# Performance work log

Measured on AMD Instinct MI355X. Metric: run time of the kernel, lower is better.

## Reference

```python
import jax, jax.numpy as jnp
import numpy as np

B, DIM, IN_DIM, H, W = 4, 512, 256, 64, 64
DOWN = IN_DIM // 2          # 128
QK = DOWN // 8              # 16
EPS = 1e-5


def conv2d(x, w, b, pad=0, dil=1):
    y = jax.lax.conv_general_dilated(
        x, w, window_strides=(1, 1),
        padding=[(pad, pad), (pad, pad)],
        rhs_dilation=(dil, dil),
        dimension_numbers=('NCHW', 'OIHW', 'NCHW'))
    return y + b[None, :, None, None]


def bn(x, g, bt, m, v):
    # inference-mode BatchNorm2d with running stats
    scale = (g * jax.lax.rsqrt(v + EPS))[None, :, None, None]
    return (x - m[None, :, None, None]) * scale + bt[None, :, None, None]


def prelu(x, a):
    return jnp.where(x >= 0, x, a * x)


def setup_inputs() -> dict:
    key = jax.random.key(0)
    ks = iter(jax.random.split(key, 64))
    d = {}
    d['x'] = jax.random.normal(next(ks), (B, DIM, H, W), dtype=jnp.float32)

    def conv_params(name, cout, cin, k):
        d[name + '_w'] = jax.random.normal(next(ks), (cout, cin, k, k), jnp.float32) * 0.05
        d[name + '_b'] = jax.random.normal(next(ks), (cout,), jnp.float32) * 0.05

    def bn_params(name, c):
        d[name + '_g'] = 1.0 + 0.1 * jax.random.normal(next(ks), (c,), jnp.float32)
        d[name + '_bt'] = 0.1 * jax.random.normal(next(ks), (c,), jnp.float32)
        d[name + '_m'] = 0.1 * jax.random.normal(next(ks), (c,), jnp.float32)
        d[name + '_v'] = 0.5 + jax.random.uniform(next(ks), (c,), jnp.float32)

    def prelu_param(name):
        d[name] = jnp.full((1,), 0.25, jnp.float32)

    conv_params('dc', IN_DIM, DIM, 3);  bn_params('dc_bn', IN_DIM); prelu_param('dc_a')
    conv_params('c1', DOWN, IN_DIM, 1); bn_params('c1_bn', DOWN);   prelu_param('c1_a')
    conv_params('c2', DOWN, IN_DIM, 3); bn_params('c2_bn', DOWN);   prelu_param('c2_a')
    conv_params('q', QK, DOWN, 1)
    conv_params('k', QK, DOWN, 1)
    conv_params('v', DOWN, DOWN, 1)
    d['gamma2'] = jnp.full((1,), 0.1, jnp.float32)  # torch init is 0; nonzero to exercise the path
    conv_params('c3', DOWN, IN_DIM, 1); bn_params('c3_bn', DOWN);   prelu_param('c3_a')
    conv_params('f', IN_DIM, 3 * DOWN, 1); bn_params('f_bn', IN_DIM); prelu_param('f_a')
    return d


def reference(x,
              dc_w, dc_b, dc_bn_g, dc_bn_bt, dc_bn_m, dc_bn_v, dc_a,
              c1_w, c1_b, c1_bn_g, c1_bn_bt, c1_bn_m, c1_bn_v, c1_a,
              c2_w, c2_b, c2_bn_g, c2_bn_bt, c2_bn_m, c2_bn_v, c2_a,
              q_w, q_b, k_w, k_b, v_w, v_b, gamma2,
              c3_w, c3_b, c3_bn_g, c3_bn_bt, c3_bn_m, c3_bn_v, c3_a,
              f_w, f_b, f_bn_g, f_bn_bt, f_bn_m, f_bn_v, f_a):
    # down_conv: 3x3 conv + BN + PReLU
    x = prelu(bn(conv2d(x, dc_w, dc_b, pad=1), dc_bn_g, dc_bn_bt, dc_bn_m, dc_bn_v), dc_a)
    # branch 1: 1x1 conv
    c1 = prelu(bn(conv2d(x, c1_w, c1_b), c1_bn_g, c1_bn_bt, c1_bn_m, c1_bn_v), c1_a)
    # branch 2: dilated 3x3 conv + non-local self-attention
    c2 = prelu(bn(conv2d(x, c2_w, c2_b, pad=2, dil=2), c2_bn_g, c2_bn_bt, c2_bn_m, c2_bn_v), c2_a)
    b, c, h, w = c2.shape
    hw = h * w
    q = conv2d(c2, q_w, q_b).reshape(b, QK, hw)   # [B, C/8, HW]
    k = conv2d(c2, k_w, k_b).reshape(b, QK, hw)
    v = conv2d(c2, v_w, v_b).reshape(b, c, hw)
    energy = jnp.einsum('bcn,bcm->bnm', q, k)     # [B, HW, HW]
    attn = jax.nn.softmax(energy, axis=-1)
    out2 = jnp.einsum('bcm,bnm->bcn', v, attn).reshape(b, c, h, w)
    out2 = gamma2 * out2 + c2
    # branch 3: global avg pool -> 1x1 conv -> broadcast (bilinear upsample of 1x1 is constant)
    pooled = jnp.mean(x, axis=(2, 3), keepdims=True)  # [B, IN_DIM, 1, 1]
    c3 = prelu(bn(conv2d(pooled, c3_w, c3_b), c3_bn_g, c3_bn_bt, c3_bn_m, c3_bn_v), c3_a)
    c3 = jnp.broadcast_to(c3, (b, DOWN, h, w))
    # fuse
    cat = jnp.concatenate([c1, out2, c3], axis=1)
    return prelu(bn(conv2d(cat, f_w, f_b), f_bn_g, f_bn_bt, f_bn_m, f_bn_v), f_a)
```

## Files before the change

kernel.cpp:

```cpp
#include <hip/hip_runtime.h>
#include <hip/hip_bf16.h>
#include <math.h>

#define HW 4096
#define EPSV 1e-5f

typedef unsigned short ushort;
typedef __attribute__((ext_vector_type(8))) short bf16x8;
typedef __attribute__((ext_vector_type(4))) float f32x4;

__device__ inline ushort f2bf(float f) {
    __hip_bfloat16 h = __float2bfloat16(f);
    return *reinterpret_cast<ushort*>(&h);
}
__device__ inline float bf2f(ushort u) {
    unsigned int v = ((unsigned int)u) << 16;
    return __uint_as_float(v);
}

template<int C>
__global__ __launch_bounds__(256) void to_chlast_bf16(
    const float* __restrict__ src, ushort* __restrict__ dst)
{
    const int b = blockIdx.z, c0 = blockIdx.y * 64, p0 = blockIdx.x * 64;
    const int tid = threadIdx.x;
    __shared__ float sT[64][65];
    for (int i = tid; i < 4096; i += 256) {
        const int ch = i >> 6, px = i & 63;
        sT[ch][px] = src[(size_t)(b * C + c0 + ch) * HW + p0 + px];
    }
    __syncthreads();
    const int px = tid >> 2, seg = tid & 3;
    ushort tmp[16];
    #pragma unroll
    for (int j = 0; j < 16; ++j) tmp[j] = f2bf(sT[seg * 16 + j][px]);
    ushort* d = dst + (size_t)(b * HW + p0 + px) * C + c0 + seg * 16;
    *(uint4*)d = *(uint4*)&tmp[0];
    *(uint4*)(d + 8) = *(uint4*)&tmp[8];
}

__global__ __launch_bounds__(256) void dc_combine(
    const float* __restrict__ part,
    const float* __restrict__ bias, const float* __restrict__ bng,
    const float* __restrict__ bnb, const float* __restrict__ bnm,
    const float* __restrict__ bnv, const float* __restrict__ al,
    ushort* __restrict__ dst)
{
    const int b = blockIdx.z, c0 = blockIdx.y * 64, p0 = blockIdx.x * 64;
    const int tid = threadIdx.x;
    __shared__ float sT[64][65];
    __shared__ float sSc[64], sSh[64];
    if (tid < 64) {
        const int c = c0 + tid;
        const float sc = bng[c] * rsqrtf(bnv[c] + EPSV);
        sSc[tid] = sc;
        sSh[tid] = (bias[c] - bnm[c]) * sc + bnb[c];
    }
    __syncthreads();
    const float a = al[0];
    for (int i = tid; i < 4096; i += 256) {
        const int ch = i >> 6, px = i & 63;
        const size_t i0 = (size_t)(b * 256 + c0 + ch) * HW + p0 + px;
        float v = part[i0] + part[i0 + (size_t)4 * 256 * HW];
        float t = v * sSc[ch] + sSh[ch];
        sT[ch][px] = t >= 0.f ? t : a * t;
    }
    __syncthreads();
    const int px = tid >> 2, seg = tid & 3;
    ushort tmp[16];
    #pragma unroll
    for (int j = 0; j < 16; ++j) tmp[j] = f2bf(sT[seg * 16 + j][px]);
    ushort* d = dst + (size_t)(b * HW + p0 + px) * 256 + c0 + seg * 16;
    *(uint4*)d = *(uint4*)&tmp[0];
    *(uint4*)(d + 8) = *(uint4*)&tmp[8];
}

template<int KS>
__global__ __launch_bounds__(256) void c2_combine(
    const float* __restrict__ part,
    const float* __restrict__ bias, const float* __restrict__ bng,
    const float* __restrict__ bnb, const float* __restrict__ bnm,
    const float* __restrict__ bnv, const float* __restrict__ al,
    float* __restrict__ out)
{
    const int c = blockIdx.y, b = blockIdx.z;
    const int px = blockIdx.x * 1024 + threadIdx.x * 4;
    const float sc = bng[c] * rsqrtf(bnv[c] + EPSV);
    const float sh = (bias[c] - bnm[c]) * sc + bnb[c];
    const float a = al[0];
    const size_t i0 = (size_t)(b * 128 + c) * HW + px;
    float4 s = {0.f, 0.f, 0.f, 0.f};
    #pragma unroll
    for (int k = 0; k < KS; ++k) {
        const float4 v = *(const float4*)&part[i0 + (size_t)k * 4 * 128 * HW];
        s.x += v.x; s.y += v.y; s.z += v.z; s.w += v.w;
    }
    float4 o;
    float t;
    t = s.x * sc + sh; o.x = t >= 0.f ? t : a * t;
    t = s.y * sc + sh; o.y = t >= 0.f ? t : a * t;
    t = s.z * sc + sh; o.z = t >= 0.f ? t : a * t;
    t = s.w * sc + sh; o.w = t >= 0.f ? t : a * t;
    *(float4*)&out[(size_t)(b * 128 + c) * HW + px] = o;
}

template<int CIN, int COUT>
__global__ __launch_bounds__(256) void pack_w3x3(
    const float* __restrict__ w, ushort* __restrict__ wpk)
{
    const int idx = blockIdx.x * 256 + threadIdx.x;
    constexpr int total = 9 * (CIN / 32) * COUT * 32;
    if (idx >= total) return;
    const int ci_in = idx & 31;
    int rest = idx >> 5;
    const int co = rest % COUT; rest /= COUT;
    const int cc = rest % (CIN / 32);
    const int tap = rest / (CIN / 32);
    wpk[idx] = f2bf(w[((size_t)co * CIN + cc * 32 + ci_in) * 9 + tap]);
}

__global__ __launch_bounds__(256) void pack_w1x1(
    const float* __restrict__ w, ushort* __restrict__ o,
    int K, int stride, int total)
{
    const int idx = blockIdx.x * 256 + threadIdx.x;
    if (idx >= total) return;
    const int co = idx / K, k = idx - co * K;
    o[idx] = f2bf(w[(size_t)co * stride + k]);
}

template<int CIN, int COUT, int COTILE, int DIL, int ROWS, int KS>
__global__ __launch_bounds__(256, 2) void conv3x3_mfma(
    const ushort* __restrict__ xin,
    const ushort* __restrict__ wpk,
    float* __restrict__ outp)
{
    constexpr int HR = ROWS + 2 * DIL;
    constexpr int NC = 64 + 2 * DIL;
    constexpr int MT = COTILE / 16;
    constexpr int WPR = 4 / ROWS;
    constexpr int NT = ROWS;
    constexpr int SAS = 40;
    constexpr int NCO = COUT / COTILE;
    constexpr int CH = CIN / 32 / KS;
    constexpr int NA = HR * NC * 4;
    constexpr int NREG = (NA + 255) / 256;
    constexpr int WCH = 9 * MT * 64;
    constexpr int WPT = (WCH + 255) / 256;

    const int tid = threadIdx.x;
    const int wave = tid >> 6, lane = tid & 63;
    const int l15 = lane & 15, quad = lane >> 4;
    const int b = blockIdx.z;
    const int cob = blockIdx.y % NCO;
    const int ks = blockIdx.y / NCO;
    const int co0 = cob * COTILE;
    const int h0 = blockIdx.x * ROWS;
    const int row = wave / WPR;
    const int ntbase = (wave % WPR) * NT;

    __shared__ __align__(16) ushort sA[HR * NC * SAS];
    __shared__ __align__(16) ushort sW[WCH * 8];

    f32x4 acc[MT][NT];
    #pragma unroll
    for (int mt = 0; mt < MT; ++mt)
        #pragma unroll
        for (int nt = 0; nt < NT; ++nt) acc[mt][nt] = (f32x4){0.f, 0.f, 0.f, 0.f};

    uint4 xreg[NREG];
    uint4 wreg[WPT];

    auto loadx = [&](int cc) {
        #pragma unroll
        for (int k = 0; k < NREG; ++k) {
            const int i = tid + k * 256;
            uint4 val = {0u, 0u, 0u, 0u};
            if (i < NA) {
                const int p = i >> 2, seg = i & 3;
                const int r = p / NC, c = p - r * NC;
                const int grow = h0 - DIL + r, gcol = c - DIL;
                if (grow >= 0 && grow < 64 && gcol >= 0 && gcol < 64)
                    val = *(const uint4*)&xin[((size_t)(b * 64 + grow) * 64 + gcol) * CIN
                                              + cc * 32 + seg * 8];
            }
            xreg[k] = val;
        }
    };
    auto loadw = [&](int cc) {
        #pragma unroll
        for (int k = 0; k < WPT; ++k) {
            const int i = tid + k * 256;
            if (i < WCH) {
                const int tap = i / (MT * 64);
                const int r = i - tap * (MT * 64);
                const int mt = r >> 6, n = r & 63;
                wreg[k] = *(const uint4*)&wpk[
                    ((size_t)(tap * (CIN / 32) + cc) * COUT + co0 + mt * 16 + (n & 15)) * 32
                    + (n >> 4) * 8];
            }
        }
    };

    loadx(ks * CH);
    loadw(ks * CH);

    #pragma unroll 1
    for (int cc = ks * CH; cc < (ks + 1) * CH; ++cc) {
        if (cc != ks * CH) __syncthreads();
        #pragma unroll
        for (int k = 0; k < NREG; ++k) {
            const int i = tid + k * 256;
            if (i < NA) *(uint4*)&sA[(i >> 2) * SAS + (i & 3) * 8] = xreg[k];
        }
        #pragma unroll
        for (int k = 0; k < WPT; ++k) {
            const int i = tid + k * 256;
            if (i < WCH) *(uint4*)&sW[i * 8] = wreg[k];
        }
        __syncthreads();

        if (cc + 1 < (ks + 1) * CH) {
            loadx(cc + 1);
            loadw(cc + 1);
        }

        #pragma unroll
        for (int tap = 0; tap < 9; ++tap) {
            const int ty = tap / 3, tx = tap - ty * 3;
            const int rl = row + ty * DIL;
            bf16x8 wf[MT];
            #pragma unroll
            for (int mt = 0; mt < MT; ++mt)
                wf[mt] = *(const bf16x8*)&sW[((tap * MT + mt) * 64 + lane) * 8];
            #pragma unroll
            for (int nt = 0; nt < NT; ++nt) {
                const int cl = (ntbase + nt) * 16 + l15 + tx * DIL;
                const bf16x8 bp = *(const bf16x8*)&sA[(rl * NC + cl) * SAS + quad * 8];
                #pragma unroll
                for (int mt = 0; mt < MT; ++mt)
                    acc[mt][nt] = __builtin_amdgcn_mfma_f32_16x16x32_bf16(
                        wf[mt], bp, acc[mt][nt], 0, 0, 0);
            }
        }
    }

    #pragma unroll
    for (int mt = 0; mt < MT; ++mt)
        #pragma unroll
        for (int rr = 0; rr < 4; ++rr) {
            const int co = co0 + mt * 16 + quad * 4 + rr;
            #pragma unroll
            for (int nt = 0; nt < NT; ++nt)
                outp[((size_t)((ks * 4 + b) * COUT + co) * 64 + h0 + row) * 64
                     + (ntbase + nt) * 16 + l15] = acc[mt][nt][rr];
        }
}

template<int CIN, int COUT, bool BNACT, int OMODE>
__global__ __launch_bounds__(256) void gemm1x1_cl(
    const ushort* __restrict__ xin,
    const ushort* __restrict__ wbf,
    const float* __restrict__ bias, const float* __restrict__ bng,
    const float* __restrict__ bnb, const float* __restrict__ bnm,
    const float* __restrict__ bnv, const float* __restrict__ al,
    const float* __restrict__ ebias, void* __restrict__ outv,
    int ostride, int ocol)
{
    const int tid = threadIdx.x;
    const int wave = tid >> 6, lane = tid & 63;
    const int l15 = lane & 15, quad = lane >> 4;
    const int pix0 = blockIdx.x * 128 + wave * 32;
    const int co0 = blockIdx.y * 64;

    f32x4 acc[4][2];
    #pragma unroll
    for (int mt = 0; mt < 4; ++mt)
        #pragma unroll
        for (int nt = 0; nt < 2; ++nt) acc[mt][nt] = (f32x4){0.f, 0.f, 0.f, 0.f};

    #pragma unroll 2
    for (int cc = 0; cc < CIN / 32; ++cc) {
        bf16x8 aw[4], bp[2];
        #pragma unroll
        for (int mt = 0; mt < 4; ++mt)
            aw[mt] = *(const bf16x8*)&wbf[(size_t)(co0 + mt * 16 + l15) * CIN + cc * 32 + quad * 8];
        #pragma unroll
        for (int nt = 0; nt < 2; ++nt)
            bp[nt] = *(const bf16x8*)&xin[(size_t)(pix0 + nt * 16 + l15) * CIN + cc * 32 + quad * 8];
        #pragma unroll
        for (int mt = 0; mt < 4; ++mt)
            #pragma unroll
            for (int nt = 0; nt < 2; ++nt)
                acc[mt][nt] = __builtin_amdgcn_mfma_f32_16x16x32_bf16(
                    aw[mt], bp[nt], acc[mt][nt], 0, 0, 0);
    }

    const int bI = pix0 >> 12;
    const float a = BNACT ? al[0] : 0.f;

    if (OMODE == 0) {
        float* out = (float*)outv;
        #pragma unroll
        for (int mt = 0; mt < 4; ++mt)
            #pragma unroll
            for (int r = 0; r < 4; ++r) {
                const int co = co0 + mt * 16 + quad * 4 + r;
                float bb = bias[co];
                if (ebias) bb += ebias[bI * COUT + co];
                float scale = 1.f, shift = bb;
                if (BNACT) {
                    scale = bng[co] * rsqrtf(bnv[co] + EPSV);
                    shift = bb * scale + (bnb[co] - bnm[co] * scale);
                }
                #pragma unroll
                for (int nt = 0; nt < 2; ++nt) {
                    float t = acc[mt][nt][r] * scale + shift;
                    if (BNACT) t = t >= 0.f ? t : a * t;
                    out[((size_t)(bI * COUT + co)) * HW + (pix0 & 4095) + nt * 16 + l15] = t;
                }
            }
    } else {
        __shared__ ushort sT[4][32][68];
        #pragma unroll
        for (int mt = 0; mt < 4; ++mt)
            #pragma unroll
            for (int r = 0; r < 4; ++r) {
                const int co = co0 + mt * 16 + quad * 4 + r;
                float bb = bias[co];
                float scale = 1.f, shift = bb;
                if (BNACT) {
                    scale = bng[co] * rsqrtf(bnv[co] + EPSV);
                    shift = bb * scale + (bnb[co] - bnm[co] * scale);
                }
                #pragma unroll
                for (int nt = 0; nt < 2; ++nt) {
                    float t = acc[mt][nt][r] * scale + shift;
                    if (BNACT) t = t >= 0.f ? t : a * t;
                    sT[wave][nt * 16 + l15][mt * 16 + quad * 4 + r] = f2bf(t);
                }
            }
        __syncthreads();
        const int p = lane >> 1, half = lane & 1;
        ushort* out = (ushort*)outv;
        #pragma unroll
        for (int seg = 0; seg < 4; ++seg) {
            uint2 a0 = *(uint2*)&sT[wave][p][half * 32 + seg * 8];
            uint2 a1 = *(uint2*)&sT[wave][p][half * 32 + seg * 8 + 4];
            uint4 vv = {a0.x, a0.y, a1.x, a1.y};
            *(uint4*)&out[(size_t)(pix0 + p) * ostride + ocol + co0 + half * 32 + seg * 8] = vv;
        }
    }
}

template<int CIN, bool BNACT, bool OUTBF16>
__global__ __launch_bounds__(256) void conv1x1_kernel(
    const float* __restrict__ in0,
    const float* __restrict__ wgt, int wstride, int COUT,
    const float* __restrict__ bias, const float* __restrict__ al,
    void* __restrict__ outv)
{
    const int tid = threadIdx.x;
    const int b = blockIdx.z, co0 = blockIdx.y * 64, p0 = blockIdx.x * 64;
    const int cg = tid >> 4, pg = tid & 15;
    const int c0l = cg * 4, w0 = pg * 4;

    __shared__ __align__(16) float sIn[16 * 64];
    __shared__ __align__(16) float sW[16 * 68];

    float acc[4][4] = {};

    for (int cc = 0; cc < CIN; cc += 16) {
        {
            int i = tid;
            #pragma unroll
            for (int it = 0; it < 4; ++it, i += 256) {
                const int px = i & 63, ci = i >> 6;
                sIn[ci * 64 + px] = in0[(size_t)(b * CIN + cc + ci) * HW + p0 + px];
            }
            i = tid;
            #pragma unroll
            for (int it = 0; it < 4; ++it, i += 256) {
                const int ci = i & 15, co = i >> 4;
                sW[ci * 68 + co] = wgt[(co0 + co) * wstride + cc + ci];
            }
        }
        __syncthreads();
        #pragma unroll
        for (int ci = 0; ci < 16; ++ci) {
            const float4 iv = *(const float4*)&sIn[ci * 64 + w0];
            const float4 wv = *(const float4*)&sW[ci * 68 + c0l];
            const float ia[4] = {iv.x, iv.y, iv.z, iv.w};
            const float wa[4] = {wv.x, wv.y, wv.z, wv.w};
            #pragma unroll
            for (int i2 = 0; i2 < 4; ++i2)
                #pragma unroll
                for (int j = 0; j < 4; ++j)
                    acc[i2][j] = fmaf(wa[i2], ia[j], acc[i2][j]);
        }
        __syncthreads();
    }

    const float a = BNACT ? al[0] : 0.f;
    #pragma unroll
    for (int i2 = 0; i2 < 4; ++i2) {
        const int co = co0 + c0l + i2;
        const float shift = bias[co];
        float r[4];
        #pragma unroll
        for (int j = 0; j < 4; ++j) {
            float t = acc[i2][j] + shift;
            r[j] = (BNACT && t < 0.f) ? a * t : t;
        }
        const size_t base = (size_t)(b * COUT + co) * HW + p0 + w0;
        if (OUTBF16) {
            ushort* out = (ushort*)outv;
            #pragma unroll
            for (int j = 0; j < 4; ++j) out[base + j] = f2bf(r[j]);
        } else {
            float* out = (float*)outv;
            *(float4*)&out[base] = make_float4(r[0], r[1], r[2], r[3]);
        }
    }
}

__global__ __launch_bounds__(256) void qk_kernel(
    const float* __restrict__ c2g, const float* __restrict__ qw,
    const float* __restrict__ qb2, const float* __restrict__ kw,
    const float* __restrict__ kb2, ushort* __restrict__ qpack,
    ushort* __restrict__ kpack)
{
    const int b = blockIdx.y, p0 = blockIdx.x * 64, tid = threadIdx.x;
    __shared__ float sC[128][64];
    __shared__ float sWq[16][128];
    __shared__ float sWk[16][128];
    for (int i = tid; i < 8192; i += 256) {
        const int px = i & 63, ci = i >> 6;
        sC[ci][px] = c2g[(size_t)(b * 128 + ci) * HW + p0 + px];
    }
    for (int i = tid; i < 2048; i += 256) {
        const int ci = i & 127, co = i >> 7;
        sWq[co][ci] = qw[co * 128 + ci];
        sWk[co][ci] = kw[co * 128 + ci];
    }
    __syncthreads();
    const int px = tid & 63, grp = tid >> 6;
    const int co0 = (grp & 1) * 8;
    const bool isK = grp >= 2;
    const float* sWp = isK ? &sWk[0][0] : &sWq[0][0];
    float acc[8] = {};
    for (int ci = 0; ci < 128; ++ci) {
        const float xv = sC[ci][px];
        #pragma unroll
        for (int j = 0; j < 8; ++j)
            acc[j] = fmaf(sWp[(co0 + j) * 128 + ci], xv, acc[j]);
    }
    const float* bsrc = isK ? kb2 : qb2;
    ushort* osrc = isK ? kpack : qpack;
    const size_t base = (size_t)(b * 4096 + p0 + px) * 32;
    #pragma unroll
    for (int j = 0; j < 8; ++j) {
        osrc[base + co0 + j] = f2bf(acc[j] + bsrc[co0 + j]);
        osrc[base + 16 + co0 + j] = 0;
    }
}

__global__ __launch_bounds__(256) void attn_flash(
    const ushort* __restrict__ qpack,
    const ushort* __restrict__ kpack,
    const ushort* __restrict__ vpackT,
    ushort* __restrict__ opart,
    float* __restrict__ Mpart,
    float* __restrict__ Spart)
{
    const int tid = threadIdx.x;
    const int wave = tid >> 6, lane = tid & 63;
    const int l15 = lane & 15, quad = lane >> 4;
    const int b = blockIdx.z, j = blockIdx.y;
    const int n0w = blockIdx.x * 128 + wave * 32;
    const int m_begin = j * 512;

    __shared__ __align__(16) ushort sV[2][128][40];
    __shared__ __align__(16) ushort sP[4][2][16][40];

    const bf16x8 bq0 = *(const bf16x8*)(qpack + ((size_t)(b * 4096 + n0w + l15) * 32 + quad * 8));
    const bf16x8 bq1 = *(const bf16x8*)(qpack + ((size_t)(b * 4096 + n0w + 16 + l15) * 32 + quad * 8));
    const f32x4 z = {0.f, 0.f, 0.f, 0.f};

    float runM0 = -3e30f, runM1 = -3e30f;
    #pragma unroll 2
    for (int t = 0; t < 8; ++t) {
        const int m0 = m_begin + t * 64;
        #pragma unroll
        for (int ms = 0; ms < 4; ++ms) {
            const bf16x8 ak = *(const bf16x8*)(
                kpack + ((size_t)(b * 4096 + m0 + ms * 16 + l15) * 32 + quad * 8));
            const f32x4 s0 = __builtin_amdgcn_mfma_f32_16x16x32_bf16(ak, bq0, z, 0, 0, 0);
            const f32x4 s1 = __builtin_amdgcn_mfma_f32_16x16x32_bf16(ak, bq1, z, 0, 0, 0);
            runM0 = fmaxf(runM0, fmaxf(fmaxf(s0[0], s0[1]), fmaxf(s0[2], s0[3])));
            runM1 = fmaxf(runM1, fmaxf(fmaxf(s1[0], s1[1]), fmaxf(s1[2], s1[3])));
        }
    }
    runM0 = fmaxf(runM0, __shfl_xor(runM0, 16));
    runM0 = fmaxf(runM0, __shfl_xor(runM0, 32));
    runM1 = fmaxf(runM1, __shfl_xor(runM1, 16));
    runM1 = fmaxf(runM1, __shfl_xor(runM1, 32));
    const float Ms0 = runM0 * 1.44269504f;
    const float Ms1 = runM1 * 1.44269504f;

    float runS0 = 0.f, runS1 = 0.f;
    f32x4 oacc0[8], oacc1[8];
    #pragma unroll
    for (int cs = 0; cs < 8; ++cs) {
        oacc0[cs] = (f32x4){0.f, 0.f, 0.f, 0.f};
        oacc1[cs] = (f32x4){0.f, 0.f, 0.f, 0.f};
    }

    const int stc = tid >> 1, stseg = tid & 1;

    {
        uint4 v0 = *(const uint4*)&vpackT[(size_t)(b * 128 + stc) * HW + m_begin + stseg * 16];
        uint4 v1 = *(const uint4*)&vpackT[(size_t)(b * 128 + stc) * HW + m_begin + stseg * 16 + 8];
        *(uint4*)&sV[0][stc][stseg * 16] = v0;
        *(uint4*)&sV[0][stc][stseg * 16 + 8] = v1;
    }
    __syncthreads();

    #pragma unroll 1
    for (int t = 0; t < 16; ++t) {
        const int m0 = m_begin + t * 32;
        const int buf = t & 1;
        uint4 nv0, nv1;
        const bool more = (t + 1 < 16);
        if (more) {
            const size_t nb = (size_t)(b * 128 + stc) * HW + m0 + 32 + stseg * 16;
            nv0 = *(const uint4*)&vpackT[nb];
            nv1 = *(const uint4*)&vpackT[nb + 8];
        }
        f32x4 s0[2], s1[2];
        #pragma unroll
        for (int ms = 0; ms < 2; ++ms) {
            const bf16x8 ak = *(const bf16x8*)(
                kpack + ((size_t)(b * 4096 + m0 + ms * 16 + l15) * 32 + quad * 8));
            s0[ms] = __builtin_amdgcn_mfma_f32_16x16x32_bf16(ak, bq0, z, 0, 0, 0);
            s1[ms] = __builtin_amdgcn_mfma_f32_16x16x32_bf16(ak, bq1, z, 0, 0, 0);
        }
        #pragma unroll
        for (int ms = 0; ms < 2; ++ms) {
            float p0[4], p1[4];
            #pragma unroll
            for (int r = 0; r < 4; ++r) {
                p0[r] = __builtin_amdgcn_exp2f(fmaf(s0[ms][r], 1.44269504f, -Ms0));
                p1[r] = __builtin_amdgcn_exp2f(fmaf(s1[ms][r], 1.44269504f, -Ms1));
                runS0 += p0[r];
                runS1 += p1[r];
            }
            ushort4 u0, u1;
            u0.x = f2bf(p0[0]); u0.y = f2bf(p0[1]); u0.z = f2bf(p0[2]); u0.w = f2bf(p0[3]);
            u1.x = f2bf(p1[0]); u1.y = f2bf(p1[1]); u1.z = f2bf(p1[2]); u1.w = f2bf(p1[3]);
            *(uint2*)&sP[wave][0][l15][ms * 16 + quad * 4] = *(uint2*)&u0;
            *(uint2*)&sP[wave][1][l15][ms * 16 + quad * 4] = *(uint2*)&u1;
        }
        asm volatile("s_waitcnt lgkmcnt(0)" ::: "memory");
        const bf16x8 ap0 = *(const bf16x8*)&sP[wave][0][l15][quad * 8];
        const bf16x8 ap1 = *(const bf16x8*)&sP[wave][1][l15][quad * 8];
        #pragma unroll
        for (int cs = 0; cs < 8; ++cs) {
            const bf16x8 bv = *(const bf16x8*)&sV[buf][cs * 16 + l15][quad * 8];
            oacc0[cs] = __builtin_amdgcn_mfma_f32_16x16x32_bf16(ap0, bv, oacc0[cs], 0, 0, 0);
            oacc1[cs] = __builtin_amdgcn_mfma_f32_16x16x32_bf16(ap1, bv, oacc1[cs], 0, 0, 0);
        }
        if (more) {
            *(uint4*)&sV[buf ^ 1][stc][stseg * 16] = nv0;
            *(uint4*)&sV[buf ^ 1][stc][stseg * 16 + 8] = nv1;
            __syncthreads();
        }
    }

    runS0 += __shfl_xor(runS0, 16);
    runS0 += __shfl_xor(runS0, 32);
    runS1 += __shfl_xor(runS1, 16);
    runS1 += __shfl_xor(runS1, 32);
    if (lane < 32) {
        const float Mv = (lane < 16) ? runM0 : runM1;
        const float Sv = (lane < 16) ? runS0 : runS1;
        const int n = n0w + ((lane < 16) ? 0 : 16) + l15;
        Mpart[((size_t)b * 8 + j) * 4096 + n] = Mv;
        Spart[((size_t)b * 8 + j) * 4096 + n] = Sv;
    }
    #pragma unroll
    for (int cs = 0; cs < 8; ++cs)
        #pragma unroll
        for (int r = 0; r < 4; ++r) {
            const int n = n0w + quad * 4 + r;
            opart[(((size_t)b * 8 + j) * 4096 + n) * 128 + cs * 16 + l15] = f2bf(oacc0[cs][r]);
            opart[(((size_t)b * 8 + j) * 4096 + n + 16) * 128 + cs * 16 + l15] = f2bf(oacc1[cs][r]);
        }
}

__global__ __launch_bounds__(256) void attn_combine(
    const ushort* __restrict__ opart, const float* __restrict__ Mpart,
    const float* __restrict__ Spart, const float* __restrict__ c2g,
    const float* __restrict__ gamma2, ushort* __restrict__ catb)
{
    const int b = blockIdx.y, n0 = blockIdx.x * 32, tid = threadIdx.x;
    __shared__ float sC2[128][33];
    __shared__ float sWj[8][32];
    if (tid < 32) {
        const int n = n0 + tid;
        float Mj[8], Sj[8];
        #pragma unroll
        for (int j = 0; j < 8; ++j) {
            Mj[j] = Mpart[((size_t)b * 8 + j) * 4096 + n];
            Sj[j] = Spart[((size_t)b * 8 + j) * 4096 + n];
        }
        float M = -3e30f;
        #pragma unroll
        for (int j = 0; j < 8; ++j) M = fmaxf(M, Mj[j]);
        float St = 0.f, e[8];
        #pragma unroll
        for (int j = 0; j < 8; ++j) { e[j] = __expf(Mj[j] - M); St += Sj[j] * e[j]; }
        const float inv = 1.0f / St;
        #pragma unroll
        for (int j = 0; j < 8; ++j) sWj[j][tid] = e[j] * inv;
    }
    #pragma unroll
    for (int e = 0; e < 16; ++e) {
        const int idx = tid + e * 256;
        const int c = idx >> 5, n = idx & 31;
        sC2[c][n] = c2g[(size_t)(b * 128 + c) * HW + n0 + n];
    }
    __syncthreads();
    const float g2 = gamma2[0];
    #pragma unroll
    for (int e = 0; e < 16; ++e) {
        const int idx = tid + e * 256;
        const int n = idx >> 7, c = idx & 127;
        float s = 0.f;
        #pragma unroll
        for (int j = 0; j < 8; ++j)
            s += bf2f(opart[(((size_t)b * 8 + j) * 4096 + n0 + n) * 128 + c]) * sWj[j][n];
        catb[(size_t)(b * 4096 + n0 + n) * 256 + 128 + c] = f2bf(fmaf(g2, s, sC2[c][n]));
    }
}

__global__ __launch_bounds__(256) void pool_kernel(
    const float* __restrict__ part,
    const float* __restrict__ bias, const float* __restrict__ bng,
    const float* __restrict__ bnb, const float* __restrict__ bnm,
    const float* __restrict__ bnv, const float* __restrict__ al,
    float* __restrict__ pool)
{
    const int c = blockIdx.x, b = blockIdx.y, tid = threadIdx.x;
    const float sc = bng[c] * rsqrtf(bnv[c] + EPSV);
    const float sh = (bias[c] - bnm[c]) * sc + bnb[c];
    const float a = al[0];
    const float4* r0 = (const float4*)(part + (size_t)(b * 256 + c) * HW);
    const float4* r1 = (const float4*)(part + (size_t)((4 + b) * 256 + c) * HW);
    float s = 0.f;
    #pragma unroll 4
    for (int i = tid; i < 1024; i += 256) {
        const float4 t0 = r0[i];
        const float4 t1 = r1[i];
        float v, t;
        v = t0.x + t1.x; t = v * sc + sh; s += t >= 0.f ? t : a * t;
        v = t0.y + t1.y; t = v * sc + sh; s += t >= 0.f ? t : a * t;
        v = t0.z + t1.z; t = v * sc + sh; s += t >= 0.f ? t : a * t;
        v = t0.w + t1.w; t = v * sc + sh; s += t >= 0.f ? t : a * t;
    }
    __shared__ float red[256];
    red[tid] = s; __syncthreads();
    for (int st = 128; st > 0; st >>= 1) {
        if (tid < st) red[tid] += red[tid + st];
        __syncthreads();
    }
    if (tid == 0) pool[b * 256 + c] = red[0] * (1.0f / 4096.0f);
}

__global__ __launch_bounds__(256) void c3_fbias_kernel(
    const float* __restrict__ pool, const float* __restrict__ c3w,
    const float* __restrict__ c3b, const float* __restrict__ bng,
    const float* __restrict__ bnb, const float* __restrict__ bnm,
    const float* __restrict__ bnv, const float* __restrict__ al,
    const float* __restrict__ fw, float* __restrict__ fbias)
{
    const int b = blockIdx.x, tid = threadIdx.x;
    __shared__ float sp[256];
    __shared__ float sc3[128];
    sp[tid] = pool[b * 256 + tid];
    __syncthreads();
    if (tid < 128) {
        float acc = c3b[tid];
        for (int ci = 0; ci < 256; ++ci) acc = fmaf(c3w[tid * 256 + ci], sp[ci], acc);
        const float scale = bng[tid] * rsqrtf(bnv[tid] + EPSV);
        float t = (acc - bnm[tid]) * scale + bnb[tid];
        const float a = al[0];
        sc3[tid] = t >= 0.f ? t : a * t;
    }
    __syncthreads();
    float f = 0.f;
    for (int j = 0; j < 128; ++j) f = fmaf(fw[tid * 384 + 256 + j], sc3[j], f);
    fbias[b * 256 + tid] = f;
}

extern "C" void kernel_launch(void* const* d_in, const int* in_sizes, int n_in,
                              void* d_out, int out_size, void* d_ws, size_t ws_size,
                              hipStream_t stream)
{
    const float* x     = (const float*)d_in[0];
    const float* dc_w  = (const float*)d_in[1];
    const float* dc_b  = (const float*)d_in[2];
    const float* dc_g  = (const float*)d_in[3];
    const float* dc_bt = (const float*)d_in[4];
    const float* dc_m  = (const float*)d_in[5];
    const float* dc_v  = (const float*)d_in[6];
    const float* dc_a  = (const float*)d_in[7];
    const float* c1_w  = (const float*)d_in[8];
    const float* c1_b  = (const float*)d_in[9];
    const float* c1_g  = (const float*)d_in[10];
    const float* c1_bt = (const float*)d_in[11];
    const float* c1_m  = (const float*)d_in[12];
    const float* c1_v  = (const float*)d_in[13];
    const float* c1_a  = (const float*)d_in[14];
    const float* c2_w  = (const float*)d_in[15];
    const float* c2_b  = (const float*)d_in[16];
    const float* c2_g  = (const float*)d_in[17];
    const float* c2_bt = (const float*)d_in[18];
    const float* c2_m  = (const float*)d_in[19];
    const float* c2_v  = (const float*)d_in[20];
    const float* c2_a  = (const float*)d_in[21];
    const float* q_w   = (const float*)d_in[22];
    const float* q_b   = (const float*)d_in[23];
    const float* k_w   = (const float*)d_in[24];
    const float* k_b   = (const float*)d_in[25];
    const float* v_w   = (const float*)d_in[26];
    const float* v_b   = (const float*)d_in[27];
    const float* gamma2= (const float*)d_in[28];
    const float* c3_w  = (const float*)d_in[29];
    const float* c3_b  = (const float*)d_in[30];
    const float* c3_g  = (const float*)d_in[31];
    const float* c3_bt = (const float*)d_in[32];
    const float* c3_m  = (const float*)d_in[33];
    const float* c3_v  = (const float*)d_in[34];
    const float* c3_a  = (const float*)d_in[35];
    const float* f_w   = (const float*)d_in[36];
    const float* f_b   = (const float*)d_in[37];
    const float* f_g   = (const float*)d_in[38];
    const float* f_bt  = (const float*)d_in[39];
    const float* f_m   = (const float*)d_in[40];
    const float* f_v   = (const float*)d_in[41];
    const float* f_a   = (const float*)d_in[42];

    char* base = (char*)d_ws;
    ushort* xbf   = (ushort*)base;
    float*  dcp   = (float*)(base + 16777216);
    float*  c2p   = (float*)base;
    ushort* opart = (ushort*)base;
    ushort* qpk   = (ushort*)(base + 33554432);
    ushort* kpk   = (ushort*)(base + 34603008);
    ushort* vbh   = (ushort*)(base + 35651584);
    ushort* xpbf  = (ushort*)(base + 50331648);
    float*  c2b   = (float*)(base + 50331648);
    ushort* catb  = (ushort*)(base + 58720256);
    ushort* wdcp  = (ushort*)(base + 75497472);
    ushort* wc2p  = (ushort*)(base + 77856768);
    ushort* wc1b  = (ushort*)(base + 78446592);
    ushort* wfb   = (ushort*)(base + 78512128);
    float*  poolb = (float*)(base + 78643200);
    float*  fbb   = (float*)(base + 78647296);
    float*  Mpart = (float*)(base + 78651392);
    float*  Spart = (float*)(base + 79175680);

    pack_w3x3<512, 256><<<dim3((9*16*256*32 + 255)/256), 256, 0, stream>>>(dc_w, wdcp);
    pack_w3x3<256, 128><<<dim3((9*8*128*32 + 255)/256), 256, 0, stream>>>(c2_w, wc2p);
    pack_w1x1<<<dim3((32768 + 255)/256), 256, 0, stream>>>(c1_w, wc1b, 256, 256, 32768);
    pack_w1x1<<<dim3((65536 + 255)/256), 256, 0, stream>>>(f_w, wfb, 256, 384, 65536);
    to_chlast_bf16<512><<<dim3(64, 8, 4), 256, 0, stream>>>(x, xbf);
    conv3x3_mfma<512, 256, 64, 1, 4, 2><<<dim3(16, 8, 4), 256, 0, stream>>>(
        xbf, wdcp, dcp);
    dc_combine<<<dim3(64, 4, 4), 256, 0, stream>>>(
        dcp, dc_b, dc_g, dc_bt, dc_m, dc_v, dc_a, xpbf);
    pool_kernel<<<dim3(256, 4), 256, 0, stream>>>(
        dcp, dc_b, dc_g, dc_bt, dc_m, dc_v, dc_a, poolb);
    c3_fbias_kernel<<<dim3(4), 256, 0, stream>>>(
        poolb, c3_w, c3_b, c3_g, c3_bt, c3_m, c3_v, c3_a, f_w, fbb);
    gemm1x1_cl<256, 128, true, 1><<<dim3(128, 2), 256, 0, stream>>>(
        xpbf, wc1b, c1_b, c1_g, c1_bt, c1_m, c1_v, c1_a, nullptr, catb, 256, 0);
    conv3x3_mfma<256, 128, 64, 2, 4, 4><<<dim3(16, 8, 4), 256, 0, stream>>>(
        xpbf, wc2p, c2p);
    c2_combine<4><<<dim3(4, 128, 4), 256, 0, stream>>>(
        c2p, c2_b, c2_g, c2_bt, c2_m, c2_v, c2_a, c2b);
    qk_kernel<<<dim3(64, 4), 256, 0, stream>>>(c2b, q_w, q_b, k_w, k_b, qpk, kpk);
    conv1x1_kernel<128, false, true><<<dim3(64, 2, 4), 256, 0, stream>>>(
        c2b, v_w, 128, 128, v_b, nullptr, vbh);
    attn_flash<<<dim3(32, 8, 4), 256, 0, stream>>>(qpk, kpk, vbh, opart, Mpart, Spart);
    attn_combine<<<dim3(128, 4), 256, 0, stream>>>(opart, Mpart, Spart, c2b, gamma2, catb);
    gemm1x1_cl<256, 256, true, 0><<<dim3(128, 4), 256, 0, stream>>>(
        catb, wfb, f_b, f_g, f_bt, f_m, f_v, f_a, fbb, (float*)d_out, 0, 0);
}
```

Before: 418.6 us.

## Fuse BN/PReLU/pool epilogues into 3x3 convs and drop split-K partials

The split-K partial-sum outputs of both 3x3 convolutions are removed. BN, PReLU, bf16 channel-last transpose (via shared memory) and global average-pool accumulation (via atomics) now run directly in the conv epilogue. This eliminates the dc_combine, pool_kernel and c2_combine launches and their large fp32 partial-buffer traffic. In exchange each block loops over the full input-channel range, so tiles shrink (COTILE 32, ROWS 2) to keep enough blocks in flight. The change also adds atomic adds for the pool and raises occupancy hints for the first conv.

```diff
diff --git a/kernel.cpp b/kernel.cpp
--- a/kernel.cpp
+++ b/kernel.cpp
@@ -37,71 +37,6 @@
     ushort* d = dst + (size_t)(b * HW + p0 + px) * C + c0 + seg * 16;
     *(uint4*)d = *(uint4*)&tmp[0];
     *(uint4*)(d + 8) = *(uint4*)&tmp[8];
-}
-
-__global__ __launch_bounds__(256) void dc_combine(
-    const float* __restrict__ part,
-    const float* __restrict__ bias, const float* __restrict__ bng,
-    const float* __restrict__ bnb, const float* __restrict__ bnm,
-    const float* __restrict__ bnv, const float* __restrict__ al,
-    ushort* __restrict__ dst)
-{
-    const int b = blockIdx.z, c0 = blockIdx.y * 64, p0 = blockIdx.x * 64;
-    const int tid = threadIdx.x;
-    __shared__ float sT[64][65];
-    __shared__ float sSc[64], sSh[64];
-    if (tid < 64) {
-        const int c = c0 + tid;
-        const float sc = bng[c] * rsqrtf(bnv[c] + EPSV);
-        sSc[tid] = sc;
-        sSh[tid] = (bias[c] - bnm[c]) * sc + bnb[c];
-    }
-    __syncthreads();
-    const float a = al[0];
-    for (int i = tid; i < 4096; i += 256) {
-        const int ch = i >> 6, px = i & 63;
-        const size_t i0 = (size_t)(b * 256 + c0 + ch) * HW + p0 + px;
-        float v = part[i0] + part[i0 + (size_t)4 * 256 * HW];
-        float t = v * sSc[ch] + sSh[ch];
-        sT[ch][px] = t >= 0.f ? t : a * t;
-    }
-    __syncthreads();
-    const int px = tid >> 2, seg = tid & 3;
-    ushort tmp[16];
-    #pragma unroll
-    for (int j = 0; j < 16; ++j) tmp[j] = f2bf(sT[seg * 16 + j][px]);
-    ushort* d = dst + (size_t)(b * HW + p0 + px) * 256 + c0 + seg * 16;
-    *(uint4*)d = *(uint4*)&tmp[0];
-    *(uint4*)(d + 8) = *(uint4*)&tmp[8];
-}
-
-template<int KS>
-__global__ __launch_bounds__(256) void c2_combine(
-    const float* __restrict__ part,
-    const float* __restrict__ bias, const float* __restrict__ bng,
-    const float* __restrict__ bnb, const float* __restrict__ bnm,
-    const float* __restrict__ bnv, const float* __restrict__ al,
-    float* __restrict__ out)
-{
-    const int c = blockIdx.y, b = blockIdx.z;
-    const int px = blockIdx.x * 1024 + threadIdx.x * 4;
-    const float sc = bng[c] * rsqrtf(bnv[c] + EPSV);
-    const float sh = (bias[c] - bnm[c]) * sc + bnb[c];
-    const float a = al[0];
-    const size_t i0 = (size_t)(b * 128 + c) * HW + px;
-    float4 s = {0.f, 0.f, 0.f, 0.f};
-    #pragma unroll
-    for (int k = 0; k < KS; ++k) {
-        const float4 v = *(const float4*)&part[i0 + (size_t)k * 4 * 128 * HW];
-        s.x += v.x; s.y += v.y; s.z += v.z; s.w += v.w;
-    }
-    float4 o;
-    float t;
-    t = s.x * sc + sh; o.x = t >= 0.f ? t : a * t;
-    t = s.y * sc + sh; o.y = t >= 0.f ? t : a * t;
-    t = s.z * sc + sh; o.z = t >= 0.f ? t : a * t;
-    t = s.w * sc + sh; o.w = t >= 0.f ? t : a * t;
-    *(float4*)&out[(size_t)(b * 128 + c) * HW + px] = o;
 }
 
 template<int CIN, int COUT>
@@ -129,11 +64,20 @@
     o[idx] = f2bf(w[(size_t)co * stride + k]);
 }
 
-template<int CIN, int COUT, int COTILE, int DIL, int ROWS, int KS>
-__global__ __launch_bounds__(256, 2) void conv3x3_mfma(
+__global__ __launch_bounds__(256) void zero_pool(float* __restrict__ p)
+{
+    p[blockIdx.x * 256 + threadIdx.x] = 0.f;
+}
+
+template<int CIN, int COUT, int COTILE, int DIL, int ROWS, int OMODE>
+__global__ __launch_bounds__(256, OMODE == 0 ? 4 : 2) void conv3x3_fused(
     const ushort* __restrict__ xin,
     const ushort* __restrict__ wpk,
-    float* __restrict__ outp)
+    const float* __restrict__ bias, const float* __restrict__ bng,
+    const float* __restrict__ bnb, const float* __restrict__ bnm,
+    const float* __restrict__ bnv, const float* __restrict__ al,
+    void* __restrict__ outv,
+    float* __restrict__ pool)
 {
     constexpr int HR = ROWS + 2 * DIL;
     constexpr int NC = 64 + 2 * DIL;
@@ -141,8 +85,7 @@
     constexpr int WPR = 4 / ROWS;
     constexpr int NT = ROWS;
     constexpr int SAS = 40;
-    constexpr int NCO = COUT / COTILE;
-    constexpr int CH = CIN / 32 / KS;
+    constexpr int CH = CIN / 32;
     constexpr int NA = HR * NC * 4;
     constexpr int NREG = (NA + 255) / 256;
     constexpr int WCH = 9 * MT * 64;
@@ -152,8 +95,7 @@
     const int wave = tid >> 6, lane = tid & 63;
     const int l15 = lane & 15, quad = lane >> 4;
     const int b = blockIdx.z;
-    const int cob = blockIdx.y % NCO;
-    const int ks = blockIdx.y / NCO;
+    const int cob = blockIdx.y;
     const int co0 = cob * COTILE;
     const int h0 = blockIdx.x * ROWS;
     const int row = wave / WPR;
@@ -202,12 +144,12 @@
         }
     };
 
-    loadx(ks * CH);
-    loadw(ks * CH);
+    loadx(0);
+    loadw(0);
 
     #pragma unroll 1
-    for (int cc = ks * CH; cc < (ks + 1) * CH; ++cc) {
-        if (cc != ks * CH) __syncthreads();
+    for (int cc = 0; cc < CH; ++cc) {
+        if (cc != 0) __syncthreads();
         #pragma unroll
         for (int k = 0; k < NREG; ++k) {
             const int i = tid + k * 256;
@@ -220,7 +162,7 @@
         }
         __syncthreads();
 
-        if (cc + 1 < (ks + 1) * CH) {
+        if (cc + 1 < CH) {
             loadx(cc + 1);
             loadw(cc + 1);
         }
@@ -245,16 +187,75 @@
         }
     }
 
-    #pragma unroll
-    for (int mt = 0; mt < MT; ++mt)
-        #pragma unroll
-        for (int rr = 0; rr < 4; ++rr) {
-            const int co = co0 + mt * 16 + quad * 4 + rr;
-            #pragma unroll
-            for (int nt = 0; nt < NT; ++nt)
-                outp[((size_t)((ks * 4 + b) * COUT + co) * 64 + h0 + row) * 64
-                     + (ntbase + nt) * 16 + l15] = acc[mt][nt][rr];
-        }
+    const float a = al[0];
+
+    if constexpr (OMODE == 0) {
+        __syncthreads();
+        ushort* sT = sA;
+        #pragma unroll
+        for (int mt = 0; mt < MT; ++mt) {
+            float sc[4], sh[4], psum[4];
+            #pragma unroll
+            for (int rr = 0; rr < 4; ++rr) {
+                const int co = co0 + mt * 16 + quad * 4 + rr;
+                sc[rr] = bng[co] * rsqrtf(bnv[co] + EPSV);
+                sh[rr] = (bias[co] - bnm[co]) * sc[rr] + bnb[co];
+                psum[rr] = 0.f;
+            }
+            #pragma unroll
+            for (int nt = 0; nt < NT; ++nt) {
+                float tv[4];
+                #pragma unroll
+                for (int rr = 0; rr < 4; ++rr) {
+                    float t = acc[mt][nt][rr] * sc[rr] + sh[rr];
+                    t = t >= 0.f ? t : a * t;
+                    tv[rr] = t;
+                    psum[rr] += t;
+                }
+                ushort4 u;
+                u.x = f2bf(tv[0]); u.y = f2bf(tv[1]);
+                u.z = f2bf(tv[2]); u.w = f2bf(tv[3]);
+                const int px = (ntbase + nt) * 16 + l15;
+                *(ushort4*)&sT[(row * 64 + px) * 40 + mt * 16 + quad * 4] = u;
+            }
+            #pragma unroll
+            for (int rr = 0; rr < 4; ++rr) {
+                float v = psum[rr];
+                v += __shfl_xor(v, 1);
+                v += __shfl_xor(v, 2);
+                v += __shfl_xor(v, 4);
+                v += __shfl_xor(v, 8);
+                if (l15 == 0)
+                    atomicAdd(&pool[b * 256 + co0 + mt * 16 + quad * 4 + rr], v);
+            }
+        }
+        __syncthreads();
+        ushort* dst = (ushort*)outv;
+        const int p = tid >> 1, half = tid & 1;
+        const uint4 v0 = *(const uint4*)&sT[p * 40 + half * 16];
+        const uint4 v1 = *(const uint4*)&sT[p * 40 + half * 16 + 8];
+        const size_t off = ((size_t)(b * 4096 + (h0 + (p >> 6)) * 64 + (p & 63))) * 256
+                           + co0 + half * 16;
+        *(uint4*)&dst[off] = v0;
+        *(uint4*)&dst[off + 8] = v1;
+    } else {
+        float* out = (float*)outv;
+        #pragma unroll
+        for (int mt = 0; mt < MT; ++mt)
+            #pragma unroll
+            for (int rr = 0; rr < 4; ++rr) {
+                const int co = co0 + mt * 16 + quad * 4 + rr;
+                const float sc = bng[co] * rsqrtf(bnv[co] + EPSV);
+                const float sh = (bias[co] - bnm[co]) * sc + bnb[co];
+                #pragma unroll
+                for (int nt = 0; nt < NT; ++nt) {
+                    float t = acc[mt][nt][rr] * sc + sh;
+                    t = t >= 0.f ? t : a * t;
+                    out[((size_t)(b * COUT + co) * 64 + h0 + row) * 64
+                        + (ntbase + nt) * 16 + l15] = t;
+                }
+            }
+    }
 }
 
 template<int CIN, int COUT, bool BNACT, int OMODE>
@@ -644,39 +645,6 @@
     }
 }
 
-__global__ __launch_bounds__(256) void pool_kernel(
-    const float* __restrict__ part,
-    const float* __restrict__ bias, const float* __restrict__ bng,
-    const float* __restrict__ bnb, const float* __restrict__ bnm,
-    const float* __restrict__ bnv, const float* __restrict__ al,
-    float* __restrict__ pool)
-{
-    const int c = blockIdx.x, b = blockIdx.y, tid = threadIdx.x;
-    const float sc = bng[c] * rsqrtf(bnv[c] + EPSV);
-    const float sh = (bias[c] - bnm[c]) * sc + bnb[c];
-    const float a = al[0];
-    const float4* r0 = (const float4*)(part + (size_t)(b * 256 + c) * HW);
-    const float4* r1 = (const float4*)(part + (size_t)((4 + b) * 256 + c) * HW);
-    float s = 0.f;
-    #pragma unroll 4
-    for (int i = tid; i < 1024; i += 256) {
-        const float4 t0 = r0[i];
-        const float4 t1 = r1[i];
-        float v, t;
-        v = t0.x + t1.x; t = v * sc + sh; s += t >= 0.f ? t : a * t;
-        v = t0.y + t1.y; t = v * sc + sh; s += t >= 0.f ? t : a * t;
-        v = t0.z + t1.z; t = v * sc + sh; s += t >= 0.f ? t : a * t;
-        v = t0.w + t1.w; t = v * sc + sh; s += t >= 0.f ? t : a * t;
-    }
-    __shared__ float red[256];
-    red[tid] = s; __syncthreads();
-    for (int st = 128; st > 0; st >>= 1) {
-        if (tid < st) red[tid] += red[tid + st];
-        __syncthreads();
-    }
-    if (tid == 0) pool[b * 256 + c] = red[0] * (1.0f / 4096.0f);
-}
-
 __global__ __launch_bounds__(256) void c3_fbias_kernel(
     const float* __restrict__ pool, const float* __restrict__ c3w,
     const float* __restrict__ c3b, const float* __restrict__ bng,
@@ -687,7 +655,7 @@
     const int b = blockIdx.x, tid = threadIdx.x;
     __shared__ float sp[256];
     __shared__ float sc3[128];
-    sp[tid] = pool[b * 256 + tid];
+    sp[tid] = pool[b * 256 + tid] * (1.0f / 4096.0f);
     __syncthreads();
     if (tid < 128) {
         float acc = c3b[tid];
@@ -753,14 +721,12 @@
 
     char* base = (char*)d_ws;
     ushort* xbf   = (ushort*)base;
-    float*  dcp   = (float*)(base + 16777216);
-    float*  c2p   = (float*)base;
     ushort* opart = (ushort*)base;
     ushort* qpk   = (ushort*)(base + 33554432);
     ushort* kpk   = (ushort*)(base + 34603008);
     ushort* vbh   = (ushort*)(base + 35651584);
+    float*  c2b   = (float*)(base + 39845888);
     ushort* xpbf  = (ushort*)(base + 50331648);
-    float*  c2b   = (float*)(base + 50331648);
     ushort* catb  = (ushort*)(base + 58720256);
     ushort* wdcp  = (ushort*)(base + 75497472);
     ushort* wc2p  = (ushort*)(base + 77856768);
@@ -776,20 +742,15 @@
     pack_w1x1<<<dim3((32768 + 255)/256), 256, 0, stream>>>(c1_w, wc1b, 256, 256, 32768);
     pack_w1x1<<<dim3((65536 + 255)/256), 256, 0, stream>>>(f_w, wfb, 256, 384, 65536);
     to_chlast_bf16<512><<<dim3(64, 8, 4), 256, 0, stream>>>(x, xbf);
-    conv3x3_mfma<512, 256, 64, 1, 4, 2><<<dim3(16, 8, 4), 256, 0, stream>>>(
-        xbf, wdcp, dcp);
-    dc_combine<<<dim3(64, 4, 4), 256, 0, stream>>>(
-        dcp, dc_b, dc_g, dc_bt, dc_m, dc_v, dc_a, xpbf);
-    pool_kernel<<<dim3(256, 4), 256, 0, stream>>>(
-        dcp, dc_b, dc_g, dc_bt, dc_m, dc_v, dc_a, poolb);
+    zero_pool<<<dim3(4), 256, 0, stream>>>(poolb);
+    conv3x3_fused<512, 256, 32, 1, 2, 0><<<dim3(32, 8, 4), 256, 0, stream>>>(
+        xbf, wdcp, dc_b, dc_g, dc_bt, dc_m, dc_v, dc_a, xpbf, poolb);
     c3_fbias_kernel<<<dim3(4), 256, 0, stream>>>(
         poolb, c3_w, c3_b, c3_g, c3_bt, c3_m, c3_v, c3_a, f_w, fbb);
     gemm1x1_cl<256, 128, true, 1><<<dim3(128, 2), 256, 0, stream>>>(
         xpbf, wc1b, c1_b, c1_g, c1_bt, c1_m, c1_v, c1_a, nullptr, catb, 256, 0);
-    conv3x3_mfma<256, 128, 64, 2, 4, 4><<<dim3(16, 8, 4), 256, 0, stream>>>(
-        xpbf, wc2p, c2p);
-    c2_combine<4><<<dim3(4, 128, 4), 256, 0, stream>>>(
-        c2p, c2_b, c2_g, c2_bt, c2_m, c2_v, c2_a, c2b);
+    conv3x3_fused<256, 128, 32, 2, 2, 1><<<dim3(32, 4, 4), 256, 0, stream>>>(
+        xpbf, wc2p, c2_b, c2_g, c2_bt, c2_m, c2_v, c2_a, c2b, nullptr);
     qk_kernel<<<dim3(64, 4), 256, 0, stream>>>(c2b, q_w, q_b, k_w, k_b, qpk, kpk);
     conv1x1_kernel<128, false, true><<<dim3(64, 2, 4), 256, 0, stream>>>(
         c2b, v_w, 128, 128, v_b, nullptr, vbh);
```

Result: slower. 460.8 us (+10.1%).
